# Kernel optimization log

Hardware: AMD Instinct MI355X
Metric: run time of the kernel (lower is better)

## Reference

```python
import jax, jax.numpy as jnp
import numpy as np

B, N, T, F_IN = 16, 1024, 12, 1
D_MODEL, D_K, D_V, H, K = 512, 32, 32, 3, 3
C = 32  # nb_chev_filter == nb_time_filter


def _ln(x, g, b, eps=1e-5):
    mu = jnp.mean(x, -1, keepdims=True)
    var = jnp.var(x, -1, keepdims=True)
    return (x - mu) * jax.lax.rsqrt(var + eps) * g + b


def _conv(x, w, b):
    y = jax.lax.conv_general_dilated(x, w, (1, 1), 'VALID',
                                     dimension_numbers=('NCHW', 'OIHW', 'NCHW'))
    return y + b[None, :, None, None]


def setup_inputs() -> dict:
    key = jax.random.key(0)
    ks = iter(jax.random.split(key, 40))
    rn = lambda s, sc=0.02: jax.random.normal(next(ks), s, jnp.float32) * sc
    return dict(
        x=rn((B, N, F_IN, T), 1.0),
        res_att=rn((B, F_IN, H, T, T), 0.1),
        pos_embed_T=rn((T, N)),
        gamma_T=jnp.ones((N,)), beta_T=jnp.zeros((N,)),
        WQ_t=rn((N, D_K * H)), WK_t=rn((N, D_K * H)), WV_t=rn((N, D_V * H)),
        fc_t=rn((H * D_V, N)),
        pre_conv_w=rn((D_MODEL, T, 1, F_IN)), pre_conv_b=rn((D_MODEL,)),
        pos_embed_S=rn((N, D_MODEL)),
        gamma_S=jnp.ones((D_MODEL,)), beta_S=jnp.zeros((D_MODEL,)),
        WQ_s=rn((D_MODEL, D_K * K)), WK_s=rn((D_MODEL, D_K * K)),
        cheb_polys=rn((K, N, N), 0.05),
        adj_pa=(jax.random.uniform(next(ks), (N, N)) < 0.01).astype(jnp.float32),
        cheb_mask=rn((K, N, N)),
        Theta=rn((K, F_IN, C), 0.1),
        gtu3_w=rn((2 * C, C, 1, 3)), gtu3_b=rn((2 * C,)),
        gtu5_w=rn((2 * C, C, 1, 5)), gtu5_b=rn((2 * C,)),
        gtu7_w=rn((2 * C, C, 1, 7)), gtu7_b=rn((2 * C,)),
        res_conv_w=rn((C, F_IN, 1, 1)), res_conv_b=rn((C,)),
        fcmy_w=rn((3 * T - 12, T)), fcmy_b=rn((T,)),
        gamma_f=jnp.ones((C,)), beta_f=jnp.zeros((C,)),
    )


def reference(x, res_att, pos_embed_T, gamma_T, beta_T, WQ_t, WK_t, WV_t, fc_t,
              pre_conv_w, pre_conv_b, pos_embed_S, gamma_S, beta_S, WQ_s, WK_s,
              cheb_polys, adj_pa, cheb_mask, Theta,
              gtu3_w, gtu3_b, gtu5_w, gtu5_b, gtu7_w, gtu7_b,
              res_conv_w, res_conv_b, fcmy_w, fcmy_b, gamma_f, beta_f):
    B_, N_, F_, T_ = x.shape
    # ---- temporal embedding (num_of_features == 1 branch): (B,F,T,N) ----
    TEmx = _ln(jnp.transpose(x, (0, 2, 3, 1)) + pos_embed_T[None, None], gamma_T, beta_T)

    # ---- temporal MHA with residual attention bias ----
    def heads(e, W, d):
        y = e @ W  # (B,F,T,H*d)
        return jnp.transpose(y.reshape(B_, F_, T_, H, d), (0, 1, 3, 2, 4))  # (B,F,H,T,d)
    Q, Kt, V = heads(TEmx, WQ_t, D_K), heads(TEmx, WK_t, D_K), heads(TEmx, WV_t, D_V)
    re_At = jnp.einsum('bfhqd,bfhkd->bfhqk', Q, Kt) / np.sqrt(D_K) + res_att
    attn = jax.nn.softmax(re_At, axis=-1)
    ctx = jnp.einsum('bfhqk,bfhkd->bfhqd', attn, V)
    ctx = jnp.transpose(ctx, (0, 1, 3, 2, 4)).reshape(B_, F_, T_, H * D_V)
    one_n, zero_n = jnp.ones((N_,), x.dtype), jnp.zeros((N_,), x.dtype)
    TATout = _ln(ctx @ fc_t + TEmx, one_n, zero_n)  # fresh LayerNorm(d_model) -> gamma=1, beta=0

    # ---- pre_conv: Conv2d(T, d_model, kernel=(1,F)) on (B,T,N,F); take last col ----
    x_TAt = jnp.einsum('btnf,dtf->bnd', jnp.transpose(TATout, (0, 2, 3, 1)),
                       pre_conv_w[:, :, 0, :]) + pre_conv_b  # (B,N,d_model)

    # ---- spatial embedding + spatial attention scores (no softmax) ----
    SEmx = _ln(x_TAt + pos_embed_S[None], gamma_S, beta_S)  # dropout = identity (eval)
    Qs = jnp.transpose((SEmx @ WQ_s).reshape(B_, N_, K, D_K), (0, 2, 1, 3))
    Ks = jnp.transpose((SEmx @ WK_s).reshape(B_, N_, K, D_K), (0, 2, 1, 3))
    STAt = jnp.einsum('bknd,bkmd->bknm', Qs, Ks) / np.sqrt(D_K)  # (B,K,N,N)

    # ---- Chebyshev graph conv weighted by spatial attention ----
    satt = jax.nn.softmax(STAt + (adj_pa[None] * cheb_mask)[None], axis=2)
    Tka = cheb_polys[None] * satt  # (B,K,N,N)
    rhs = jnp.einsum('bkmn,bmft->bknft', Tka, x)  # T_k_with_at^T @ x over all t
    spatial_gcn = jax.nn.relu(jnp.einsum('bknft,kfo->bnot', rhs, Theta))  # (B,N,C,T)

    # ---- gated temporal convs (GTU) ----
    X = jnp.transpose(spatial_gcn, (0, 2, 1, 3))  # (B,C,N,T)
    def gtu(w, b):
        y = _conv(X, w, b)
        return jnp.tanh(y[:, :C]) * jax.nn.sigmoid(y[:, C:])
    time_conv = jnp.concatenate([gtu(gtu3_w, gtu3_b), gtu(gtu5_w, gtu5_b),
                                 gtu(gtu7_w, gtu7_b)], axis=-1)  # (B,C,N,3T-12)
    time_conv = time_conv @ fcmy_w + fcmy_b  # (B,C,N,T)
    tco = jax.nn.relu(time_conv)  # num_of_features == 1 branch

    # ---- residual 1x1 conv + final LayerNorm over channel dim ----
    x_res = _conv(jnp.transpose(x, (0, 2, 1, 3)), res_conv_w, res_conv_b)  # (B,C,N,T)
    out = _ln(jnp.transpose(jax.nn.relu(x_res + tco), (0, 3, 2, 1)), gamma_f, beta_f)
    out = jnp.transpose(out, (0, 2, 3, 1))  # (B,N,C,T)
    return out, re_At
```

## Files before the change

### kernel.cpp

```cpp
#include <hip/hip_runtime.h>
#include <hip/hip_bf16.h>
#include <math.h>

#define B_ 16
#define N_ 1024
#define T_ 12
#define DM_ 512
#define H_ 3
#define K_ 3
#define C_ 32
#define RSQRT_DK 0.17677669529663687f

typedef __attribute__((ext_vector_type(8))) short bf16x8;
typedef __attribute__((ext_vector_type(4))) float f32x4;

__device__ __forceinline__ ushort f2bf(float f) {
  uint u = __float_as_uint(f);
  return (ushort)((u + 0x7FFF + ((u >> 16) & 1)) >> 16);
}

__global__ void k1_temporal_ln(const float* __restrict__ x, const float* __restrict__ posT,
                               const float* __restrict__ gT, const float* __restrict__ bT,
                               float* __restrict__ TEmx) {
  int row = blockIdx.x;
  int b = row / T_, t = row - b * T_;
  __shared__ float red[256], red2[256];
  float v[4]; float s = 0.f, s2 = 0.f;
  for (int i = 0; i < 4; ++i) {
    int n = threadIdx.x + (i << 8);
    float val = x[(b * N_ + n) * T_ + t] + posT[t * N_ + n];
    v[i] = val; s += val; s2 += val * val;
  }
  red[threadIdx.x] = s; red2[threadIdx.x] = s2;
  __syncthreads();
  for (int off = 128; off > 0; off >>= 1) {
    if (threadIdx.x < off) { red[threadIdx.x] += red[threadIdx.x + off]; red2[threadIdx.x] += red2[threadIdx.x + off]; }
    __syncthreads();
  }
  float mu = red[0] * (1.f / N_);
  float rs = rsqrtf(red2[0] * (1.f / N_) - mu * mu + 1e-5f);
  for (int i = 0; i < 4; ++i) {
    int n = threadIdx.x + (i << 8);
    TEmx[row * N_ + n] = (v[i] - mu) * rs * gT[n] + bT[n];
  }
}

__global__ __launch_bounds__(256) void k2_qkv(const float* __restrict__ TEmx,
                       const float* __restrict__ WQ, const float* __restrict__ WK,
                       const float* __restrict__ WV, float* __restrict__ part) {
  int kc = blockIdx.x, row = blockIdx.y;
  __shared__ float e[256];
  int tid = threadIdx.x;
  e[tid] = TEmx[row * N_ + kc * 256 + tid];
  __syncthreads();
  for (int col = tid; col < 288; col += 256) {
    int which = col / 96, j = col - which * 96;
    const float* W = (which == 0) ? WQ : ((which == 1) ? WK : WV);
    const float* Wp = W + (size_t)(kc * 256) * 96 + j;
    float acc = 0.f;
    #pragma unroll 8
    for (int n = 0; n < 256; ++n) acc += e[n] * Wp[n * 96];
    part[(row * 4 + kc) * 288 + col] = acc;
  }
}

__global__ void k3a_attn(const float* __restrict__ part, const float* __restrict__ res_att,
                         float* __restrict__ reAt_out, float* __restrict__ ctx) {
  int b = blockIdx.x;
  __shared__ float q_l[T_ * 288];
  __shared__ float s_l[H_ * T_ * T_];
  for (int i = threadIdx.x; i < T_ * 288; i += 256) {
    int t = i / 288, col = i - t * 288;
    const float* pr = &part[(size_t)((b * T_ + t) * 4) * 288 + col];
    q_l[i] = pr[0] + pr[288] + pr[576] + pr[864];
  }
  __syncthreads();
  for (int idx = threadIdx.x; idx < H_ * T_ * T_; idx += 256) {
    int h = idx / 144, r = idx - h * 144, qi = r / 12, ki = r - qi * 12;
    float acc = 0.f;
    #pragma unroll
    for (int d = 0; d < 32; ++d)
      acc += q_l[qi * 288 + h * 32 + d] * q_l[ki * 288 + 96 + h * 32 + d];
    float sv = acc * RSQRT_DK + res_att[(b * H_ + h) * 144 + qi * 12 + ki];
    s_l[idx] = sv;
    reAt_out[(b * H_ + h) * 144 + qi * 12 + ki] = sv;
  }
  __syncthreads();
  if (threadIdx.x < 36) {
    int h = threadIdx.x / 12, qi = threadIdx.x - h * 12;
    float mx = -1e30f;
    for (int ki = 0; ki < 12; ++ki) mx = fmaxf(mx, s_l[h * 144 + qi * 12 + ki]);
    float sum = 0.f;
    for (int ki = 0; ki < 12; ++ki) { float p = __expf(s_l[h * 144 + qi * 12 + ki] - mx); s_l[h * 144 + qi * 12 + ki] = p; sum += p; }
    float inv = 1.f / sum;
    for (int ki = 0; ki < 12; ++ki) s_l[h * 144 + qi * 12 + ki] *= inv;
  }
  __syncthreads();
  for (int idx = threadIdx.x; idx < T_ * 96; idx += 256) {
    int qi = idx / 96, hd = idx - qi * 96, h = hd >> 5, d = hd & 31;
    float acc = 0.f;
    for (int ki = 0; ki < 12; ++ki)
      acc += s_l[h * 144 + qi * 12 + ki] * q_l[ki * 288 + 192 + h * 32 + d];
    ctx[(b * T_ + qi) * 96 + hd] = acc;
  }
}

__global__ __launch_bounds__(1024) void k3b_tat(const float* __restrict__ ctx,
                        const float* __restrict__ fc_t,
                        const float* __restrict__ TEmx, float* __restrict__ TAT) {
  int row = blockIdx.x;
  __shared__ float c_l[96];
  __shared__ float red[16], red2[16];
  int tid = threadIdx.x;
  if (tid < 96) c_l[tid] = ctx[row * 96 + tid];
  __syncthreads();
  float acc = TEmx[row * N_ + tid];
  #pragma unroll 12
  for (int j = 0; j < 96; ++j) acc = fmaf(c_l[j], fc_t[j * N_ + tid], acc);
  float s = acc, s2 = acc * acc;
  #pragma unroll
  for (int off = 32; off > 0; off >>= 1) {
    s  += __shfl_xor(s, off);
    s2 += __shfl_xor(s2, off);
  }
  int w = tid >> 6;
  if ((tid & 63) == 0) { red[w] = s; red2[w] = s2; }
  __syncthreads();
  float ts = 0.f, ts2 = 0.f;
  #pragma unroll
  for (int i = 0; i < 16; ++i) { ts += red[i]; ts2 += red2[i]; }
  float mu = ts * (1.f / N_);
  float rs = rsqrtf(ts2 * (1.f / N_) - mu * mu + 1e-5f);
  TAT[row * N_ + tid] = (acc - mu) * rs;
}

__global__ void k4_preconv_ln(const float* __restrict__ TAT, const float* __restrict__ pcw,
                              const float* __restrict__ pcb, const float* __restrict__ posS,
                              const float* __restrict__ gS, const float* __restrict__ bS,
                              float* __restrict__ SEmx) {
  int bn = blockIdx.x; int b = bn >> 10, n = bn & 1023;
  __shared__ float tc[12];
  __shared__ float red[256], red2[256];
  if (threadIdx.x < 12) tc[threadIdx.x] = TAT[(b * T_ + threadIdx.x) * N_ + n];
  __syncthreads();
  float v[2]; float s = 0.f, s2 = 0.f;
  for (int i = 0; i < 2; ++i) {
    int d = threadIdx.x + (i << 8);
    float acc = pcb[d];
    #pragma unroll
    for (int t = 0; t < 12; ++t) acc += tc[t] * pcw[d * 12 + t];
    acc += posS[n * DM_ + d];
    v[i] = acc; s += acc; s2 += acc * acc;
  }
  red[threadIdx.x] = s; red2[threadIdx.x] = s2;
  __syncthreads();
  for (int off = 128; off > 0; off >>= 1) {
    if (threadIdx.x < off) { red[threadIdx.x] += red[threadIdx.x + off]; red2[threadIdx.x] += red2[threadIdx.x + off]; }
    __syncthreads();
  }
  float mu = red[0] * (1.f / DM_);
  float rs = rsqrtf(red2[0] * (1.f / DM_) - mu * mu + 1e-5f);
  for (int i = 0; i < 2; ++i) {
    int d = threadIdx.x + (i << 8);
    SEmx[bn * DM_ + d] = (v[i] - mu) * rs * gS[d] + bS[d];
  }
}

__global__ void k5_pre(const float* __restrict__ WQs, const float* __restrict__ WKs,
                       ushort* __restrict__ wpre) {
  int idx = blockIdx.x * 256 + threadIdx.x;
  int k = idx / 192, col = idx - k * 192;
  float v = (col < 96) ? WQs[k * 96 + col] : WKs[k * 96 + (col - 96)];
  wpre[col * 512 + k] = f2bf(v);
}

__global__ __launch_bounds__(256) void k5_qks(const float* __restrict__ SEmx,
                                              const ushort* __restrict__ wpre,
                                              __hip_bfloat16* __restrict__ Qs,
                                              __hip_bfloat16* __restrict__ Ks) {
  int b = blockIdx.y, n0 = blockIdx.x * 32;
  __shared__ __align__(16) ushort SE_h[32 * 520];
  int tid = threadIdx.x;
  for (int idx = tid; idx < 4096; idx += 256) {
    int r = idx >> 7, cq = idx & 127;
    float4 v = *(const float4*)&SEmx[((size_t)((b << 10) + n0 + r)) * DM_ + cq * 4];
    uint lo = (uint)f2bf(v.x) | ((uint)f2bf(v.y) << 16);
    uint hi = (uint)f2bf(v.z) | ((uint)f2bf(v.w) << 16);
    *(uint2*)&SE_h[r * 520 + cq * 4] = make_uint2(lo, hi);
  }
  __syncthreads();

  int w = tid >> 6, lane = tid & 63, quad = lane >> 4, c16 = lane & 15;
  f32x4 acc[3][2];
  #pragma unroll
  for (int mi = 0; mi < 3; ++mi)
    #pragma unroll
    for (int nt = 0; nt < 2; ++nt) acc[mi][nt] = (f32x4){0.f, 0.f, 0.f, 0.f};

  for (int ks = 0; ks < 16; ++ks) {
    bf16x8 Bf0 = *(const bf16x8*)&SE_h[(0 * 16 + c16) * 520 + ks * 32 + quad * 8];
    bf16x8 Bf1 = *(const bf16x8*)&SE_h[(1 * 16 + c16) * 520 + ks * 32 + quad * 8];
    #pragma unroll
    for (int mi = 0; mi < 3; ++mi) {
      int m = (w * 3 + mi) * 16 + c16;
      bf16x8 Af = *(const bf16x8*)&wpre[m * 512 + ks * 32 + quad * 8];
      acc[mi][0] = __builtin_amdgcn_mfma_f32_16x16x32_bf16(Af, Bf0, acc[mi][0], 0, 0, 0);
      acc[mi][1] = __builtin_amdgcn_mfma_f32_16x16x32_bf16(Af, Bf1, acc[mi][1], 0, 0, 0);
    }
  }
  #pragma unroll
  for (int mi = 0; mi < 3; ++mi) {
    int mb = (w * 3 + mi) * 16;
    #pragma unroll
    for (int nt = 0; nt < 2; ++nt) {
      int node = n0 + nt * 16 + c16;
      #pragma unroll
      for (int r = 0; r < 4; ++r) {
        int m = mb + quad * 4 + r;
        int j = (m < 96) ? m : m - 96;
        int kk = j >> 5, dd = j & 31;
        __hip_bfloat16* o = (m < 96) ? Qs : Ks;
        o[(((b * K_ + kk) * N_) + node) * 32 + dd] = __float2bfloat16(acc[mi][nt][r]);
      }
    }
  }
}

__global__ void k6_pre(const float* __restrict__ adj, const float* __restrict__ mask,
                       const float* __restrict__ cheb, uint* __restrict__ pk) {
  int idx = blockIdx.x * 256 + threadIdx.x;
  int mn = idx & (N_ * N_ - 1);
  uint lo = f2bf(adj[mn] * mask[idx]);
  uint hi = f2bf(cheb[idx]);
  pk[idx] = lo | (hi << 16);
}

__global__ __launch_bounds__(256) void k6_spatial(
    const __hip_bfloat16* __restrict__ Qs, const __hip_bfloat16* __restrict__ Ks,
    const uint* __restrict__ pk, const float* __restrict__ x,
    float* __restrict__ rhs) {
  const int b  = blockIdx.x;
  const int k  = blockIdx.y;
  const int n0 = blockIdx.z * 32;
  const ushort* Qb = (const ushort*)(Qs + (size_t)((b * K_ + k) * N_) * 32);
  const ushort* Kb = (const ushort*)(Ks + (size_t)((b * K_ + k) * N_) * 32);
  const uint* pkk = pk + (size_t)k * (N_ * N_);
  const float*  xb  = x + b * N_ * T_;

  __shared__ __align__(16) ushort Q_lh[64 * 32];
  __shared__ __align__(16) ushort K_lh[32 * 32];
  __shared__ __align__(16) float  x_l[64 * 12];
  __shared__ float s_l[64 * 36];
  __shared__ float pm[4 * 32], ps[4 * 32];
  __shared__ float mu[32], ell[32], fac[32], inv[32];
  __shared__ float red[8 * 32 * 12];

  const int tid  = threadIdx.x;
  const int w    = tid >> 6, lane = tid & 63;
  const int quad = lane >> 4, c16 = lane & 15;
  const int mg   = tid >> 5, nn = tid & 31;

  if (tid < 128) *(uint4*)(&K_lh[tid * 8]) = *(const uint4*)(Kb + (size_t)n0 * 32 + tid * 8);
  if (tid < 32) { mu[tid] = -1e30f; ell[tid] = 0.f; }
  float accp[12];
  #pragma unroll
  for (int t = 0; t < 12; ++t) accp[t] = 0.f;
  __syncthreads();

  for (int m0 = 0; m0 < N_; m0 += 64) {
    *(uint4*)(&Q_lh[tid * 8]) = *(const uint4*)(Qb + (size_t)m0 * 32 + tid * 8);
    if (tid < 192) *(float4*)(&x_l[tid * 4]) = *(const float4*)(xb + m0 * 12 + tid * 4);
    __syncthreads();

    bf16x8 afrag = *(const bf16x8*)(&Q_lh[(w * 16 + c16) * 32 + quad * 8]);
    f32x4 sc[2];
    float am[2][4], ch[2][4];
    #pragma unroll
    for (int ns = 0; ns < 2; ++ns) {
      bf16x8 bfrag = *(const bf16x8*)(&K_lh[(ns * 16 + c16) * 32 + quad * 8]);
      f32x4 z = {0.f, 0.f, 0.f, 0.f};
      sc[ns] = __builtin_amdgcn_mfma_f32_16x16x32_bf16(afrag, bfrag, z, 0, 0, 0);
      #pragma unroll
      for (int r = 0; r < 4; ++r) {
        int m = m0 + w * 16 + quad * 4 + r;
        uint p2 = pkk[(size_t)m * N_ + n0 + ns * 16 + c16];
        am[ns][r] = __uint_as_float(p2 << 16);
        ch[ns][r] = __uint_as_float(p2 & 0xFFFF0000u);
      }
    }
    float sv[2][4];
    #pragma unroll
    for (int ns = 0; ns < 2; ++ns) {
      float cmax = -1e30f;
      #pragma unroll
      for (int r = 0; r < 4; ++r) {
        sv[ns][r] = sc[ns][r] * RSQRT_DK + am[ns][r];
        cmax = fmaxf(cmax, sv[ns][r]);
      }
      cmax = fmaxf(cmax, __shfl_xor(cmax, 16));
      cmax = fmaxf(cmax, __shfl_xor(cmax, 32));
      if (lane < 16) pm[w * 32 + ns * 16 + lane] = cmax;
    }
    __syncthreads();
    if (tid < 32) {
      float tm = fmaxf(fmaxf(pm[tid], pm[32 + tid]), fmaxf(pm[64 + tid], pm[96 + tid]));
      float nm = fmaxf(mu[tid], tm);
      fac[tid] = __expf(mu[tid] - nm);
      mu[tid] = nm;
    }
    __syncthreads();
    {
      float f = fac[nn];
      #pragma unroll
      for (int t = 0; t < 12; ++t) accp[t] *= f;
    }
    #pragma unroll
    for (int ns = 0; ns < 2; ++ns) {
      float mcol = mu[ns * 16 + c16];
      float psum = 0.f;
      #pragma unroll
      for (int r = 0; r < 4; ++r) {
        float p = __expf(sv[ns][r] - mcol);
        psum += p;
        s_l[(w * 16 + quad * 4 + r) * 36 + ns * 16 + c16] = p * ch[ns][r];
      }
      psum += __shfl_xor(psum, 16);
      psum += __shfl_xor(psum, 32);
      if (lane < 16) ps[w * 32 + ns * 16 + lane] = psum;
    }
    __syncthreads();
    if (tid < 32)
      ell[tid] = ell[tid] * fac[tid] + ps[tid] + ps[32 + tid] + ps[64 + tid] + ps[96 + tid];
    #pragma unroll
    for (int mi = 0; mi < 8; ++mi) {
      int m = mg * 8 + mi;
      float pv = s_l[m * 36 + nn];
      const float* xr = &x_l[m * 12];
      #pragma unroll
      for (int t = 0; t < 12; ++t) accp[t] = fmaf(pv, xr[t], accp[t]);
    }
    __syncthreads();
  }
  if (tid < 32) inv[tid] = 1.f / ell[tid];
  #pragma unroll
  for (int t = 0; t < 12; ++t) red[(mg * 32 + nn) * 12 + t] = accp[t];
  __syncthreads();
  for (int idx = tid; idx < 384; idx += 256) {
    int n = idx / 12, t = idx - n * 12;
    float s = 0.f;
    #pragma unroll
    for (int g = 0; g < 8; ++g) s += red[(g * 32 + n) * 12 + t];
    rhs[((size_t)(b * K_ + k) * N_ + n0 + n) * 12 + t] = s * inv[n];
  }
}

template<int KS, int JV, int JB>
__device__ __forceinline__ void conv_mfma(const ushort* X_th, const ushort* wl_h,
                                          ushort* tc_h, const float* bias0,
                                          int mp, int ntg, int quad, int c16) {
  f32x4 accA[3], accB[3];
  #pragma unroll
  for (int i = 0; i < 3; ++i) { accA[i] = (f32x4){0.f,0.f,0.f,0.f}; accB[i] = (f32x4){0.f,0.f,0.f,0.f}; }
  #pragma unroll
  for (int dt = 0; dt < KS; ++dt) {
    bf16x8 A0 = *(const bf16x8*)&wl_h[dt * 2560 + (mp * 16 + c16) * 40 + quad * 8];
    bf16x8 A1 = *(const bf16x8*)&wl_h[dt * 2560 + ((mp + 2) * 16 + c16) * 40 + quad * 8];
    #pragma unroll
    for (int i = 0; i < 3; ++i) {
      int nt = ntg * 3 + i;
      int j = nt >> 1, sh = nt & 1;
      bf16x8 Bf = *(const bf16x8*)&X_th[(sh * 16 + c16) * 584 + (j + dt) * 32 + quad * 8];
      accA[i] = __builtin_amdgcn_mfma_f32_16x16x32_bf16(A0, Bf, accA[i], 0, 0, 0);
      accB[i] = __builtin_amdgcn_mfma_f32_16x16x32_bf16(A1, Bf, accB[i], 0, 0, 0);
    }
  }
  #pragma unroll
  for (int i = 0; i < 3; ++i) {
    int nt = ntg * 3 + i, j = nt >> 1, sh = nt & 1;
    if (j < JV) {
      int s = sh * 16 + c16;
      #pragma unroll
      for (int r = 0; r < 4; ++r) {
        int cc = mp * 16 + quad * 4 + r;
        float a = accA[i][r] + bias0[cc];
        float g = accB[i][r] + bias0[cc + 32];
        float e2a = __expf(2.f * a);
        float th = 1.f - 2.f / (e2a + 1.f);
        float sg = 1.f / (1.f + __expf(-g));
        tc_h[(s * 32 + cc) * 32 + (JB + j)] = f2bf(th * sg);
      }
    }
  }
}

__global__ __launch_bounds__(1024) void k8_fused(
                       const float* __restrict__ rhs, const float* __restrict__ Theta,
                       const float* __restrict__ x, const float* __restrict__ rw,
                       const float* __restrict__ rb,
                       const float* __restrict__ w3, const float* __restrict__ b3,
                       const float* __restrict__ w5, const float* __restrict__ b5,
                       const float* __restrict__ w7, const float* __restrict__ b7,
                       const float* __restrict__ fw, const float* __restrict__ fb,
                       const float* __restrict__ gf, const float* __restrict__ bf,
                       float* __restrict__ out) {
  int bn0 = blockIdx.x * 32;
  int b = bn0 >> 10, n0 = bn0 & 1023;

  __shared__ __align__(16) char uR[73216];
  ushort* X_th = (ushort*)uR;
  ushort* wl_h = (ushort*)(uR + 37376);
  float*  v_l  = (float*)uR;
  __shared__ __align__(16) ushort tc_h[1024 * 32];
  __shared__ float rhs_l[32 * 36];
  __shared__ float Th_l[96];
  __shared__ float xr_l[32 * 12];
  __shared__ float fw_l[288];
  __shared__ float fb_l[12];
  __shared__ float bias_l[3][64];
  __shared__ float rw_l[32], rb_l[32], gf_l[32], bf_l[32];
  __shared__ float stm[384], str[384];

  int tid = threadIdx.x;
  int w = tid >> 6, lane = tid & 63, quad = lane >> 4, c16 = lane & 15;
  int mp = w & 1, ntg = w >> 1;
  int c = (tid >> 3) & 31;
  int site = (tid & 7) | ((tid >> 8) << 3);

  for (int idx = tid; idx < 1152; idx += 1024) {
    int s = idx / 36, r = idx - s * 36, k = r / 12, t = r - k * 12;
    rhs_l[idx] = rhs[((size_t)(b * 3 + k) * N_ + n0 + s) * 12 + t];
  }
  if (tid < 384) xr_l[tid] = x[(size_t)(b * N_ + n0) * 12 + tid];
  if (tid < 96) Th_l[tid] = Theta[tid];
  if (tid < 288) fw_l[tid] = fw[tid];
  if (tid < 12) fb_l[tid] = fb[tid];
  if (tid < 64) { bias_l[0][tid] = b3[tid]; bias_l[1][tid] = b5[tid]; bias_l[2][tid] = b7[tid]; }
  if (tid >= 64 && tid < 96)  rw_l[tid - 64] = rw[tid - 64];
  if (tid >= 96 && tid < 128) rb_l[tid - 96] = rb[tid - 96];
  if (tid >= 128 && tid < 160) gf_l[tid - 128] = gf[tid - 128];
  if (tid >= 160 && tid < 192) bf_l[tid - 160] = bf[tid - 160];
  for (int idx = tid; idx < 64 * 32 * 3; idx += 1024) {
    int co = idx / 96, r2 = idx - co * 96, ic = r2 / 3, dt = r2 - ic * 3;
    wl_h[dt * 2560 + co * 40 + ic] = f2bf(w3[idx]);
  }
  __syncthreads();

  {
    float th0 = Th_l[c], th1 = Th_l[32 + c], th2 = Th_l[64 + c];
    const float* rs_ = &rhs_l[site * 36];
    ushort* xo = &X_th[site * 584 + c];
    #pragma unroll
    for (int t = 0; t < 12; ++t) {
      float a = rs_[t] * th0 + rs_[12 + t] * th1 + rs_[24 + t] * th2;
      xo[t * 32] = f2bf(fmaxf(a, 0.f));
    }
  }
  for (int idx = tid; idx < 32 * 6 * 32; idx += 1024) {
    int s = idx / 192, r2 = idx - s * 192, tt = r2 >> 5, ic = r2 & 31;
    X_th[s * 584 + (12 + tt) * 32 + ic] = 0;
  }
  __syncthreads();

  conv_mfma<3, 10, 0>(X_th, wl_h, tc_h, &bias_l[0][0], mp, ntg, quad, c16);
  __syncthreads();
  for (int idx = tid; idx < 64 * 32 * 5; idx += 1024) {
    int co = idx / 160, r2 = idx - co * 160, ic = r2 / 5, dt = r2 - ic * 5;
    wl_h[dt * 2560 + co * 40 + ic] = f2bf(w5[idx]);
  }
  __syncthreads();
  conv_mfma<5, 8, 10>(X_th, wl_h, tc_h, &bias_l[1][0], mp, ntg, quad, c16);
  __syncthreads();
  for (int idx = tid; idx < 64 * 32 * 7; idx += 1024) {
    int co = idx / 224, r2 = idx - co * 224, ic = r2 / 7, dt = r2 - ic * 7;
    wl_h[dt * 2560 + co * 40 + ic] = f2bf(w7[idx]);
  }
  __syncthreads();
  conv_mfma<7, 6, 18>(X_th, wl_h, tc_h, &bias_l[2][0], mp, ntg, quad, c16);
  __syncthreads();

  float tcv[24];
  {
    const ushort* tr = &tc_h[(site * 32 + c) * 32];
    #pragma unroll
    for (int j = 0; j < 24; ++j) tcv[j] = __uint_as_float(((uint)tr[j]) << 16);
  }
  float o[12];
  #pragma unroll
  for (int t = 0; t < 12; ++t) o[t] = fb_l[t];
  #pragma unroll
  for (int j = 0; j < 24; ++j) {
    const float4* fp = (const float4*)&fw_l[j * 12];
    float4 f0 = fp[0], f1 = fp[1], f2 = fp[2];
    float fr[12] = {f0.x, f0.y, f0.z, f0.w, f1.x, f1.y, f1.z, f1.w, f2.x, f2.y, f2.z, f2.w};
    #pragma unroll
    for (int t = 0; t < 12; ++t) o[t] = fmaf(tcv[j], fr[t], o[t]);
  }

  float v[12];
  {
    float rwc = rw_l[c], rbc = rb_l[c];
    const float* xs = &xr_l[site * 12];
    float* vo = &v_l[site * 388 + c * 12];
    #pragma unroll
    for (int t = 0; t < 12; ++t) {
      float xres = xs[t] * rwc + rbc;
      v[t] = fmaxf(xres + fmaxf(o[t], 0.f), 0.f);
      vo[t] = v[t];
    }
  }
  __syncthreads();
  if (tid < 384) {
    int s = tid / 12, t = tid - s * 12;
    float sm = 0.f, s2 = 0.f;
    #pragma unroll 8
    for (int cc = 0; cc < 32; ++cc) {
      float u = v_l[s * 388 + cc * 12 + t];
      sm += u; s2 += u * u;
    }
    float m = sm * (1.f / 32.f);
    stm[tid] = m;
    str[tid] = rsqrtf(s2 * (1.f / 32.f) - m * m + 1e-5f);
  }
  __syncthreads();
  {
    float gfc = gf_l[c], bfc = bf_l[c];
    const float* sm_ = &stm[site * 12];
    const float* sr_ = &str[site * 12];
    float q[12];
    #pragma unroll
    for (int t = 0; t < 12; ++t) q[t] = (v[t] - sm_[t]) * sr_[t] * gfc + bfc;
    float* op = &out[(size_t)(bn0 + site) * 384 + c * 12];
    ((float4*)op)[0] = make_float4(q[0], q[1], q[2], q[3]);
    ((float4*)op)[1] = make_float4(q[4], q[5], q[6], q[7]);
    ((float4*)op)[2] = make_float4(q[8], q[9], q[10], q[11]);
  }
}

extern "C" void kernel_launch(void* const* d_in, const int* in_sizes, int n_in,
                              void* d_out, int out_size, void* d_ws, size_t ws_size,
                              hipStream_t stream) {
  const float* x       = (const float*)d_in[0];
  const float* res_att = (const float*)d_in[1];
  const float* posT    = (const float*)d_in[2];
  const float* gT      = (const float*)d_in[3];
  const float* bT      = (const float*)d_in[4];
  const float* WQt     = (const float*)d_in[5];
  const float* WKt     = (const float*)d_in[6];
  const float* WVt     = (const float*)d_in[7];
  const float* fct     = (const float*)d_in[8];
  const float* pcw     = (const float*)d_in[9];
  const float* pcb     = (const float*)d_in[10];
  const float* posS    = (const float*)d_in[11];
  const float* gS      = (const float*)d_in[12];
  const float* bS      = (const float*)d_in[13];
  const float* WQs     = (const float*)d_in[14];
  const float* WKs     = (const float*)d_in[15];
  const float* cheb    = (const float*)d_in[16];
  const float* adj     = (const float*)d_in[17];
  const float* mask    = (const float*)d_in[18];
  const float* Theta   = (const float*)d_in[19];
  const float* w3      = (const float*)d_in[20];
  const float* b3      = (const float*)d_in[21];
  const float* w5      = (const float*)d_in[22];
  const float* b5      = (const float*)d_in[23];
  const float* w7      = (const float*)d_in[24];
  const float* b7      = (const float*)d_in[25];
  const float* rw      = (const float*)d_in[26];
  const float* rb      = (const float*)d_in[27];
  const float* fw      = (const float*)d_in[28];
  const float* fb      = (const float*)d_in[29];
  const float* gf      = (const float*)d_in[30];
  const float* bf      = (const float*)d_in[31];

  float* ws = (float*)d_ws;
  float* TEmx = ws;
  float* qkv  = TEmx + 196608;
  float* ctx  = qkv + 55296;
  float* TAT  = ctx + 18432;
  float* SEmx = TAT + 196608;
  float* Qsf  = SEmx + 8388608;
  float* Ksf  = Qsf + 1572864;
  float* rhs  = Ksf + 1572864;
  ushort* wpre = (ushort*)(rhs + 589824);
  float* part = SEmx;

  __hip_bfloat16* Qh = (__hip_bfloat16*)Qsf;
  __hip_bfloat16* Kh = (__hip_bfloat16*)Ksf;
  uint* pk = (uint*)SEmx;

  float* out  = (float*)d_out;
  float* reAt = out + 6291456;

  k5_pre<<<(DM_ * 192) / 256, 256, 0, stream>>>(WQs, WKs, wpre);
  k1_temporal_ln<<<B_ * T_, 256, 0, stream>>>(x, posT, gT, bT, TEmx);
  k2_qkv<<<dim3(4, B_ * T_), 256, 0, stream>>>(TEmx, WQt, WKt, WVt, part);
  k3a_attn<<<B_, 256, 0, stream>>>(part, res_att, reAt, ctx);
  k3b_tat<<<B_ * T_, 1024, 0, stream>>>(ctx, fct, TEmx, TAT);
  k4_preconv_ln<<<B_ * N_, 256, 0, stream>>>(TAT, pcw, pcb, posS, gS, bS, SEmx);
  k5_qks<<<dim3(N_ / 32, B_), 256, 0, stream>>>(SEmx, wpre, Qh, Kh);
  k6_pre<<<(K_ * N_ * N_) / 256, 256, 0, stream>>>(adj, mask, cheb, pk);
  k6_spatial<<<dim3(B_, K_, N_ / 32), 256, 0, stream>>>(Qh, Kh, pk, x, rhs);
  k8_fused<<<B_ * N_ / 32, 1024, 0, stream>>>(rhs, Theta, x, rw, rb,
                                              w3, b3, w5, b5, w7, b7, fw, fb, gf, bf, out);
}
```

Baseline: 370.9 us.

## Use per-wave online softmax in spatial kernel and swizzle LDS in fused conv

Rewrites the spatial attention kernel so each wave keeps its own running max, sum and accumulators in registers, with no LDS staging or block barriers inside the loop. The four wave partials are merged once at the end with a log-sum-exp rescale. Q and x are now read straight from global memory instead of through shared memory. The fused conv kernel also XOR-swizzles the tc_h LDS index and changes the v_l row stride from 388 to 391, both aimed at reducing bank conflicts. The cost is higher register pressure, since each thread holds 24 accumulators, plus redundant global loads of x.

```diff
diff --git a/kernel.cpp b/kernel.cpp
--- a/kernel.cpp
+++ b/kernel.cpp
@@ -245,112 +245,103 @@
   const ushort* Qb = (const ushort*)(Qs + (size_t)((b * K_ + k) * N_) * 32);
   const ushort* Kb = (const ushort*)(Ks + (size_t)((b * K_ + k) * N_) * 32);
   const uint* pkk = pk + (size_t)k * (N_ * N_);
-  const float*  xb  = x + b * N_ * T_;
-
-  __shared__ __align__(16) ushort Q_lh[64 * 32];
-  __shared__ __align__(16) ushort K_lh[32 * 32];
-  __shared__ __align__(16) float  x_l[64 * 12];
-  __shared__ float s_l[64 * 36];
-  __shared__ float pm[4 * 32], ps[4 * 32];
-  __shared__ float mu[32], ell[32], fac[32], inv[32];
-  __shared__ float red[8 * 32 * 12];
+  const float* xb = x + b * N_ * T_;
+
+  __shared__ float wmu[4][32], well[4][32];
+  __shared__ float wacc[4][32][12];
 
   const int tid  = threadIdx.x;
   const int w    = tid >> 6, lane = tid & 63;
   const int quad = lane >> 4, c16 = lane & 15;
-  const int mg   = tid >> 5, nn = tid & 31;
-
-  if (tid < 128) *(uint4*)(&K_lh[tid * 8]) = *(const uint4*)(Kb + (size_t)n0 * 32 + tid * 8);
-  if (tid < 32) { mu[tid] = -1e30f; ell[tid] = 0.f; }
-  float accp[12];
-  #pragma unroll
-  for (int t = 0; t < 12; ++t) accp[t] = 0.f;
-  __syncthreads();
-
-  for (int m0 = 0; m0 < N_; m0 += 64) {
-    *(uint4*)(&Q_lh[tid * 8]) = *(const uint4*)(Qb + (size_t)m0 * 32 + tid * 8);
-    if (tid < 192) *(float4*)(&x_l[tid * 4]) = *(const float4*)(xb + m0 * 12 + tid * 4);
-    __syncthreads();
-
-    bf16x8 afrag = *(const bf16x8*)(&Q_lh[(w * 16 + c16) * 32 + quad * 8]);
-    f32x4 sc[2];
-    float am[2][4], ch[2][4];
-    #pragma unroll
-    for (int ns = 0; ns < 2; ++ns) {
-      bf16x8 bfrag = *(const bf16x8*)(&K_lh[(ns * 16 + c16) * 32 + quad * 8]);
-      f32x4 z = {0.f, 0.f, 0.f, 0.f};
-      sc[ns] = __builtin_amdgcn_mfma_f32_16x16x32_bf16(afrag, bfrag, z, 0, 0, 0);
+
+  bf16x8 bfr0 = *(const bf16x8*)(Kb + (size_t)(n0 + c16) * 32 + quad * 8);
+  bf16x8 bfr1 = *(const bf16x8*)(Kb + (size_t)(n0 + 16 + c16) * 32 + quad * 8);
+
+  float mu0 = -1e30f, mu1 = -1e30f, el0 = 0.f, el1 = 0.f;
+  float acc0[12], acc1[12];
+  #pragma unroll
+  for (int t = 0; t < 12; ++t) { acc0[t] = 0.f; acc1[t] = 0.f; }
+
+  for (int s = 0; s < 16; ++s) {
+    const int m0 = s * 64 + w * 16;
+    bf16x8 af = *(const bf16x8*)(Qb + (size_t)(m0 + c16) * 32 + quad * 8);
+    f32x4 z = {0.f, 0.f, 0.f, 0.f};
+    f32x4 sc0 = __builtin_amdgcn_mfma_f32_16x16x32_bf16(af, bfr0, z, 0, 0, 0);
+    f32x4 sc1 = __builtin_amdgcn_mfma_f32_16x16x32_bf16(af, bfr1, z, 0, 0, 0);
+
+    const int mrow = m0 + quad * 4;
+    float sv0[4], sv1[4], ch0[4], ch1[4];
+    #pragma unroll
+    for (int r = 0; r < 4; ++r) {
+      uint p2 = pkk[(size_t)(mrow + r) * N_ + n0 + c16];
+      uint q2 = pkk[(size_t)(mrow + r) * N_ + n0 + 16 + c16];
+      sv0[r] = sc0[r] * RSQRT_DK + __uint_as_float(p2 << 16);
+      ch0[r] = __uint_as_float(p2 & 0xFFFF0000u);
+      sv1[r] = sc1[r] * RSQRT_DK + __uint_as_float(q2 << 16);
+      ch1[r] = __uint_as_float(q2 & 0xFFFF0000u);
+    }
+    float cm0 = fmaxf(fmaxf(sv0[0], sv0[1]), fmaxf(sv0[2], sv0[3]));
+    float cm1 = fmaxf(fmaxf(sv1[0], sv1[1]), fmaxf(sv1[2], sv1[3]));
+    cm0 = fmaxf(cm0, __shfl_xor(cm0, 16)); cm0 = fmaxf(cm0, __shfl_xor(cm0, 32));
+    cm1 = fmaxf(cm1, __shfl_xor(cm1, 16)); cm1 = fmaxf(cm1, __shfl_xor(cm1, 32));
+    float nm0 = fmaxf(mu0, cm0), nm1 = fmaxf(mu1, cm1);
+    float f0 = __expf(mu0 - nm0), f1 = __expf(mu1 - nm1);
+    mu0 = nm0; mu1 = nm1;
+    el0 *= f0; el1 *= f1;
+    #pragma unroll
+    for (int t = 0; t < 12; ++t) { acc0[t] *= f0; acc1[t] *= f1; }
+
+    float p0[4], p1[4];
+    #pragma unroll
+    for (int r = 0; r < 4; ++r) {
+      p0[r] = __expf(sv0[r] - mu0); el0 += p0[r]; p0[r] *= ch0[r];
+      p1[r] = __expf(sv1[r] - mu1); el1 += p1[r]; p1[r] *= ch1[r];
+    }
+    #pragma unroll
+    for (int r = 0; r < 4; ++r) {
+      const float4* xr = (const float4*)(xb + (size_t)(mrow + r) * 12);
+      float4 xA = xr[0], xB = xr[1], xC = xr[2];
+      float xv[12] = {xA.x, xA.y, xA.z, xA.w, xB.x, xB.y, xB.z, xB.w,
+                      xC.x, xC.y, xC.z, xC.w};
+      float px0 = p0[r], px1 = p1[r];
       #pragma unroll
-      for (int r = 0; r < 4; ++r) {
-        int m = m0 + w * 16 + quad * 4 + r;
-        uint p2 = pkk[(size_t)m * N_ + n0 + ns * 16 + c16];
-        am[ns][r] = __uint_as_float(p2 << 16);
-        ch[ns][r] = __uint_as_float(p2 & 0xFFFF0000u);
+      for (int t = 0; t < 12; ++t) {
+        acc0[t] = fmaf(px0, xv[t], acc0[t]);
+        acc1[t] = fmaf(px1, xv[t], acc1[t]);
       }
     }
-    float sv[2][4];
-    #pragma unroll
-    for (int ns = 0; ns < 2; ++ns) {
-      float cmax = -1e30f;
-      #pragma unroll
-      for (int r = 0; r < 4; ++r) {
-        sv[ns][r] = sc[ns][r] * RSQRT_DK + am[ns][r];
-        cmax = fmaxf(cmax, sv[ns][r]);
-      }
-      cmax = fmaxf(cmax, __shfl_xor(cmax, 16));
-      cmax = fmaxf(cmax, __shfl_xor(cmax, 32));
-      if (lane < 16) pm[w * 32 + ns * 16 + lane] = cmax;
-    }
-    __syncthreads();
-    if (tid < 32) {
-      float tm = fmaxf(fmaxf(pm[tid], pm[32 + tid]), fmaxf(pm[64 + tid], pm[96 + tid]));
-      float nm = fmaxf(mu[tid], tm);
-      fac[tid] = __expf(mu[tid] - nm);
-      mu[tid] = nm;
-    }
-    __syncthreads();
-    {
-      float f = fac[nn];
-      #pragma unroll
-      for (int t = 0; t < 12; ++t) accp[t] *= f;
-    }
-    #pragma unroll
-    for (int ns = 0; ns < 2; ++ns) {
-      float mcol = mu[ns * 16 + c16];
-      float psum = 0.f;
-      #pragma unroll
-      for (int r = 0; r < 4; ++r) {
-        float p = __expf(sv[ns][r] - mcol);
-        psum += p;
-        s_l[(w * 16 + quad * 4 + r) * 36 + ns * 16 + c16] = p * ch[ns][r];
-      }
-      psum += __shfl_xor(psum, 16);
-      psum += __shfl_xor(psum, 32);
-      if (lane < 16) ps[w * 32 + ns * 16 + lane] = psum;
-    }
-    __syncthreads();
-    if (tid < 32)
-      ell[tid] = ell[tid] * fac[tid] + ps[tid] + ps[32 + tid] + ps[64 + tid] + ps[96 + tid];
-    #pragma unroll
-    for (int mi = 0; mi < 8; ++mi) {
-      int m = mg * 8 + mi;
-      float pv = s_l[m * 36 + nn];
-      const float* xr = &x_l[m * 12];
-      #pragma unroll
-      for (int t = 0; t < 12; ++t) accp[t] = fmaf(pv, xr[t], accp[t]);
-    }
-    __syncthreads();
-  }
-  if (tid < 32) inv[tid] = 1.f / ell[tid];
-  #pragma unroll
-  for (int t = 0; t < 12; ++t) red[(mg * 32 + nn) * 12 + t] = accp[t];
-  __syncthreads();
-  for (int idx = tid; idx < 384; idx += 256) {
-    int n = idx / 12, t = idx - n * 12;
-    float s = 0.f;
-    #pragma unroll
-    for (int g = 0; g < 8; ++g) s += red[(g * 32 + n) * 12 + t];
-    rhs[((size_t)(b * K_ + k) * N_ + n0 + n) * 12 + t] = s * inv[n];
+  }
+
+  #pragma unroll
+  for (int off = 16; off <= 32; off <<= 1) {
+    el0 += __shfl_xor(el0, off);
+    el1 += __shfl_xor(el1, off);
+    #pragma unroll
+    for (int t = 0; t < 12; ++t) {
+      acc0[t] += __shfl_xor(acc0[t], off);
+      acc1[t] += __shfl_xor(acc1[t], off);
+    }
+  }
+  if (quad == 0) {
+    wmu[w][c16] = mu0; well[w][c16] = el0;
+    #pragma unroll
+    for (int t = 0; t < 12; ++t) wacc[w][c16][t] = acc0[t];
+  } else if (quad == 1) {
+    wmu[w][16 + c16] = mu1; well[w][16 + c16] = el1;
+    #pragma unroll
+    for (int t = 0; t < 12; ++t) wacc[w][16 + c16][t] = acc1[t];
+  }
+  __syncthreads();
+  if (tid < 384) {
+    int n = tid / 12, t = tid - n * 12;
+    float m0v = wmu[0][n], m1v = wmu[1][n], m2v = wmu[2][n], m3v = wmu[3][n];
+    float gm = fmaxf(fmaxf(m0v, m1v), fmaxf(m2v, m3v));
+    float e0 = __expf(m0v - gm), e1 = __expf(m1v - gm);
+    float e2 = __expf(m2v - gm), e3 = __expf(m3v - gm);
+    float den = well[0][n] * e0 + well[1][n] * e1 + well[2][n] * e2 + well[3][n] * e3;
+    float num = wacc[0][n][t] * e0 + wacc[1][n][t] * e1 +
+                wacc[2][n][t] * e2 + wacc[3][n][t] * e3;
+    rhs[((size_t)(b * K_ + k) * N_ + n0 + n) * 12 + t] = num / den;
   }
 }
 
@@ -379,6 +370,7 @@
     int nt = ntg * 3 + i, j = nt >> 1, sh = nt & 1;
     if (j < JV) {
       int s = sh * 16 + c16;
+      int sx = (s & 15) << 1;
       #pragma unroll
       for (int r = 0; r < 4; ++r) {
         int cc = mp * 16 + quad * 4 + r;
@@ -387,7 +379,7 @@
         float e2a = __expf(2.f * a);
         float th = 1.f - 2.f / (e2a + 1.f);
         float sg = 1.f / (1.f + __expf(-g));
-        tc_h[(s * 32 + cc) * 32 + (JB + j)] = f2bf(th * sg);
+        tc_h[((s * 32 + cc) * 32 + (JB + j)) ^ sx] = f2bf(th * sg);
       }
     }
   }
@@ -480,9 +472,11 @@
 
   float tcv[24];
   {
-    const ushort* tr = &tc_h[(site * 32 + c) * 32];
-    #pragma unroll
-    for (int j = 0; j < 24; ++j) tcv[j] = __uint_as_float(((uint)tr[j]) << 16);
+    int rb2 = (site * 32 + c) * 32;
+    int sx = (site & 15) << 1;
+    #pragma unroll
+    for (int j = 0; j < 24; ++j)
+      tcv[j] = __uint_as_float(((uint)tc_h[(rb2 + j) ^ sx]) << 16);
   }
   float o[12];
   #pragma unroll
@@ -500,7 +494,7 @@
   {
     float rwc = rw_l[c], rbc = rb_l[c];
     const float* xs = &xr_l[site * 12];
-    float* vo = &v_l[site * 388 + c * 12];
+    float* vo = &v_l[site * 391 + c * 12];
     #pragma unroll
     for (int t = 0; t < 12; ++t) {
       float xres = xs[t] * rwc + rbc;
@@ -514,7 +508,7 @@
     float sm = 0.f, s2 = 0.f;
     #pragma unroll 8
     for (int cc = 0; cc < 32; ++cc) {
-      float u = v_l[s * 388 + cc * 12 + t];
+      float u = v_l[s * 391 + cc * 12 + t];
       sm += u; s2 += u * u;
     }
     float m = sm * (1.f / 32.f);
```

New measurement: 351.3 us. 5.3% less time.
